# Performance work log

Measured on AMD Instinct MI355X. Metric: run time of the kernel, lower is better.

Reference implementation:

```python
import jax, jax.numpy as jnp
import numpy as np
import math

B, CIN, COUT, K, G, SD, H = 8, 512, 512, 3, 16, 512, 32
EPS = 1e-8


def _blur_kernel():
    k = jnp.array([1., 3., 3., 1.], dtype=jnp.float32)
    k = k[None, :] * k[:, None]
    k = k / k.sum()
    return k * 4.0  # upsample_factor ** 2


def setup_inputs() -> dict:
    key = jax.random.key(0)
    ks = jax.random.split(key, 10)
    return {
        "x": jax.random.normal(ks[0], (B, CIN, H, H), jnp.float32),
        "co": jax.random.uniform(ks[1], (1, CIN, CIN), jnp.float32),
        "style": jax.random.normal(ks[2], (B, 2 * SD), jnp.float32),
        "noise": jax.random.normal(ks[3], (B, 1, 2 * H, 2 * H), jnp.float32),
        "W": jax.random.normal(ks[4], (1, COUT, CIN, K, K), jnp.float32),
        "mb_w": jax.random.normal(ks[5], (G, SD), jnp.float32),
        "mb_b": jnp.ones((G,), jnp.float32),
        "mod_w": jax.random.normal(ks[6], (CIN, SD), jnp.float32),
        "mod_b": jnp.ones((CIN,), jnp.float32),
        "cluster": jax.random.normal(ks[7], (G, CIN), jnp.float32),
        "gate": -jnp.ones((1,), jnp.float32),
        "tmpr": -2.0 * jnp.ones((1,), jnp.float32),
        "noise_weight": jnp.zeros((1,), jnp.float32),
        "flr_bias": jnp.zeros((COUT,), jnp.float32),
    }


def _l2norm(x, axis):
    n = jnp.linalg.norm(x, axis=axis, keepdims=True)
    return x / jnp.maximum(n, 1e-12)


def reference(x, co, style, noise, W, mb_w, mb_b, mod_w, mod_b,
              cluster, gate, tmpr, noise_weight, flr_bias):
    scale = 1.0 / math.sqrt(CIN * K * K)   # GroupModulatedConv2d.scale
    lin_scale = 1.0 / math.sqrt(SD)        # EqualLinear scale (lr_mul=1)

    t = jax.nn.sigmoid(tmpr) * 5.0
    g = jax.nn.sigmoid(gate)
    S = jax.nn.sigmoid((co - g) * 50.0)                    # (1,Cin,Cin)
    cl = jax.nn.softmax(t * cluster, axis=0)               # (G,Cin)
    loss1 = jnp.sum((cl.T @ cl - jax.lax.stop_gradient(S)) ** 2)
    loss2 = jnp.sum((jnp.float32(CIN * CIN / G) - jnp.sum(S)) ** 2)
    grouped = jax.lax.stop_gradient(jnp.round(jax.nn.softmax(cl * 500.0, axis=0))) + 1e-6

    s1, s2 = style[:, :SD], style[:, SD:]
    style_base = (s1 @ (mb_w * lin_scale).T + mb_b)[:, :, None]   # (B,G,1)
    st = (s2 @ (mod_w * lin_scale).T + mod_b)[:, None, :]         # (B,1,Cin)
    tmp = _l2norm(grouped[None] * st, axis=2)                     # (B,G,Cin)
    st = jnp.sum(tmp * style_base, axis=1)                        # (B,Cin)

    w = scale * W * st[:, None, :, None, None]                    # (B,Cout,Cin,K,K)
    demod = jax.lax.rsqrt(jnp.sum(w * w, axis=(2, 3, 4)) + EPS)   # (B,Cout)
    w = w * demod[:, :, None, None, None]

    # conv_transpose2d(stride=2, pad=0, groups=B) == per-sample conv with
    # lhs_dilation=2, padding=K-1, spatially-flipped kernel.
    wf = w[:, :, :, ::-1, ::-1]

    def per_sample(xi, wi):  # xi (Cin,h,w), wi (Cout,Cin,K,K)
        return jax.lax.conv_general_dilated(
            xi[None], wi, window_strides=(1, 1),
            padding=((K - 1, K - 1), (K - 1, K - 1)), lhs_dilation=(2, 2),
            dimension_numbers=('NCHW', 'OIHW', 'NCHW'))[0]

    out = jax.vmap(per_sample)(x, wf)                             # (B,Cout,65,65)

    # Blur: upfirdn2d, pad=(1,1), depthwise 4x4 symmetric FIR kernel.
    bk = _blur_kernel()
    kdw = jnp.broadcast_to(bk[None, None], (COUT, 1, 4, 4))
    out = jax.lax.conv_general_dilated(
        out, kdw, (1, 1), ((1, 1), (1, 1)), feature_group_count=COUT,
        dimension_numbers=('NCHW', 'OIHW', 'NCHW'))                # (B,Cout,64,64)

    # Correlation of base weights (detached, fed to next layer as `co`).
    wflat = W.reshape(COUT, -1)
    wn = _l2norm(wflat, axis=1)
    co_out = jax.lax.stop_gradient((wn @ wn.T)[None])              # (1,Cout,Cout)

    # NoiseInjection + FusedLeakyReLU
    out = out + noise_weight * noise
    out = jax.nn.leaky_relu(out + flr_bias[None, :, None, None], 0.2) * math.sqrt(2.0)
    return out, co_out, loss1, loss2
```

## Files before the change

kernel.cpp:

```cpp
#include <hip/hip_runtime.h>
#include <hip/hip_bf16.h>

#define NB 8
#define LIN_SCALE 0.044194173824159216f
#define SCALE 0.014731391274719736f

typedef __attribute__((ext_vector_type(8))) short short8;
typedef __attribute__((ext_vector_type(4))) float floatx4;

static constexpr size_t O_XS   = 0;
static constexpr size_t O_OUT1 = 9469952;
static constexpr size_t O_WRT  = 44081152;
static constexpr size_t O_WB   = 48799744;
static constexpr size_t O_PG   = 53518336;
static constexpr size_t O_WSQ  = 61906944;
static constexpr size_t O_CL   = 62955520;
static constexpr size_t O_GR   = O_CL + 32768;
static constexpr size_t O_SB   = O_GR + 32768;
static constexpr size_t O_ST0  = O_SB + 1024;
static constexpr size_t O_STS  = O_ST0 + 16384;
static constexpr size_t O_ST2  = O_STS + 16384;
static constexpr size_t O_WNI  = O_ST2 + 16384;
static constexpr size_t O_DM   = O_WNI + 2048;
static constexpr size_t O_ACC  = O_DM + 16384;

static constexpr size_t OUT_CO = 16777216;
static constexpr size_t OUT_L  = 17039360;

__device__ const int c_ylim[4] = {33,33,32,32};
__device__ const int c_xlim[4] = {33,32,33,32};
__device__ const int c_ntap[4] = {4,2,2,1};
__device__ const int c_tap0[4] = {0,4,6,8};
__device__ const int c_nmb[4]  = {69,66,66,64};
__device__ const int c_cnt[4]  = {276,264,264,256};
__device__ const int c_dy[9] = {-1,-1,0,0, -1,0, 0,0, 0};
__device__ const int c_dx[9] = {-1,0,-1,0, 0,0, -1,0, 0};
__device__ const int c_ky[9] = {2,2,0,0, 2,0, 1,1, 1};
__device__ const int c_kx[9] = {2,0,2,0, 1,1, 2,0, 1};
__device__ const long c_poff[4] = {0, 4460544, 8785920, 13111296};

__device__ __forceinline__ float wave_red(float v) {
#pragma unroll
  for (int s = 32; s > 0; s >>= 1) v += __shfl_down(v, s);
  return v;
}

__device__ __forceinline__ void gl_lds16(const void* g, void* l) {
  __builtin_amdgcn_global_load_lds((const __attribute__((address_space(1))) void*)g,
                                   (__attribute__((address_space(3))) void*)l, 16, 0, 0);
}

__device__ __forceinline__ unsigned short bf16b(float f) {
  union { __hip_bfloat16 h; unsigned short u; } cv;
  cv.h = __float2bfloat16(f);
  return cv.u;
}

__device__ __forceinline__ float bfu(unsigned short u) {
  union { float f; unsigned u32; } c; c.u32 = ((unsigned)u) << 16; return c.f;
}

__device__ __forceinline__ int xcd_chunk(int lb, int cnt) {
  const int q = cnt >> 3, r = cnt & 7;
  const int c = lb & 7, i = lb >> 3;
  return (c < r) ? c*(q+1) + i : r*(q+1) + (c - r)*q + i;
}

__global__ __launch_bounds__(256) void k_big1(const float* __restrict__ W,
    float* __restrict__ wsq, float* __restrict__ wni,
    __hip_bfloat16* __restrict__ wrt, unsigned short* __restrict__ wb,
    const float* __restrict__ style, const float* __restrict__ mod_w,
    const float* __restrict__ mod_b, float* __restrict__ st0,
    const float* __restrict__ co, const float* __restrict__ gate,
    const float* __restrict__ cluster, const float* __restrict__ tmpr,
    const float* __restrict__ mb_w, const float* __restrict__ mb_b,
    float* __restrict__ gr, float* __restrict__ sb,
    float* __restrict__ pacc, __hip_bfloat16* __restrict__ xs) {
  __shared__ float sh[8192];
  __shared__ float extra[8];
  const int bid = blockIdx.x, tid = threadIdx.x;
  const int lane = tid & 63, wv = tid >> 6;
  if (bid < 512) {
    const int o = bid;
    for (int j = tid; j < 4608; j += 256) sh[j] = W[(size_t)o*4608 + j];
    __syncthreads();
    float tot = 0.f;
#pragma unroll
    for (int half = 0; half < 2; half++) {
      const int i = tid + half*256;
      float s = 0.f;
#pragma unroll
      for (int k = 0; k < 9; k++) { float w = sh[i*9 + k]; s = fmaf(w, w, s); }
      wsq[o*512 + i] = s; tot += s;
#pragma unroll
      for (int tp = 0; tp < 9; tp++)
        wrt[((size_t)tp*512 + o)*512 + i] = __float2bfloat16(sh[i*9 + c_ky[tp]*3 + c_kx[tp]]);
    }
    for (int j = tid; j < 4608; j += 256) wb[(size_t)o*4608 + j] = bf16b(sh[j]);
    tot = wave_red(tot);
    if (lane == 0) extra[wv] = tot;
    __syncthreads();
    if (tid == 0) wni[o] = 1.f / fmaxf(sqrtf(extra[0]+extra[1]+extra[2]+extra[3]), 1e-12f);
  } else if (bid < 576) {
    const int b = (bid - 512) >> 3, oc = (bid - 512) & 7;
    sh[tid] = style[b*1024 + 512 + tid];
    sh[tid + 256] = style[b*1024 + 768 + tid];
    __syncthreads();
#pragma unroll
    for (int rr = 0; rr < 16; rr++) {
      const int c = oc*64 + wv*16 + rr;
      const float* mw = mod_w + (size_t)c*512;
      float acc = 0.f;
#pragma unroll
      for (int it = 0; it < 8; it++) acc = fmaf(mw[lane + 64*it], sh[lane + 64*it], acc);
      acc = wave_red(acc);
      if (lane == 0) st0[b*512 + c] = acc*LIN_SCALE + mod_b[c];
    }
  } else if (bid < 1088) {
    const int i = bid - 576;
    const float tt = 5.f / (1.f + expf(-tmpr[0]));
    const float gg = 1.f / (1.f + expf(-gate[0]));
    for (int j = tid; j < 512; j += 256) {
      float v[16]; float m = -1e30f;
#pragma unroll
      for (int g = 0; g < 16; g++) { v[g] = tt * cluster[g*512 + j]; m = fmaxf(m, v[g]); }
      float s = 0.f;
#pragma unroll
      for (int g = 0; g < 16; g++) { v[g] = expf(v[g] - m); s += v[g]; }
      float inv = 1.f / s;
#pragma unroll
      for (int g = 0; g < 16; g++) sh[g*512 + j] = v[g] * inv;
    }
    __syncthreads();
    float cli[16];
#pragma unroll
    for (int k = 0; k < 16; k++) cli[k] = sh[k*512 + i];
    float p1 = 0.f, p2 = 0.f;
    for (int j = tid; j < 512; j += 256) {
      float d = 0.f;
#pragma unroll
      for (int k = 0; k < 16; k++) d = fmaf(cli[k], sh[k*512 + j], d);
      float S = 1.f / (1.f + expf(-50.f*(co[i*512 + j] - gg)));
      float e = d - S;
      p1 = fmaf(e, e, p1); p2 += S;
    }
    p1 = wave_red(p1); p2 = wave_red(p2);
    if (lane == 0) { extra[wv] = p1; extra[4 + wv] = p2; }
    __syncthreads();
    if (tid == 0)  pacc[i]       = extra[0]+extra[1]+extra[2]+extra[3];
    if (tid == 64) pacc[512 + i] = extra[4]+extra[5]+extra[6]+extra[7];
  } else if (bid == 1088) {
    const float tt = 5.f / (1.f + expf(-tmpr[0]));
#pragma unroll
    for (int h = 0; h < 2; h++) {
      const int c = tid + h*256;
      float v[16]; float m = -1e30f;
#pragma unroll
      for (int g = 0; g < 16; g++) { v[g] = tt * cluster[g*512 + c]; m = fmaxf(m, v[g]); }
      float s = 0.f;
#pragma unroll
      for (int g = 0; g < 16; g++) { v[g] = expf(v[g] - m); s += v[g]; }
      float inv = 1.f / s;
      float clv[16]; float m2 = -1e30f;
#pragma unroll
      for (int g = 0; g < 16; g++) { clv[g] = v[g]*inv; m2 = fmaxf(m2, 500.f*clv[g]); }
      float s2 = 0.f; float e2[16];
#pragma unroll
      for (int g = 0; g < 16; g++) { e2[g] = expf(500.f*clv[g] - m2); s2 += e2[g]; }
      float i2 = 1.f / s2;
#pragma unroll
      for (int g = 0; g < 16; g++) gr[g*512 + c] = rintf(e2[g]*i2) + 1e-6f;
    }
    for (int task = wv; task < 128; task += 4) {
      int b = task >> 4, g = task & 15;
      const float* s1 = style + b*1024;
      const float* mw = mb_w + g*512;
      float acc = 0.f;
#pragma unroll
      for (int it = 0; it < 8; it++) acc = fmaf(s1[lane + 64*it], mw[lane + 64*it], acc);
      acc = wave_red(acc);
      if (lane == 0) sb[b*16 + g] = acc*LIN_SCALE + mb_b[g];
    }
  } else {
    const int id0 = (bid - 1089)*256 + tid;
    const float4 z = make_float4(0.f, 0.f, 0.f, 0.f);
    float4* xq = (float4*)xs;
#pragma unroll
    for (int it = 0; it < 22; ++it) {
      const int id = id0 + it*3072;
      const int c = id & 63;
      const int pb = id >> 6;
      const int b = pb / 132;
      const int pix = pb - b*132;
      int y, xx;
      if (pix < 34)       { y = 0;        xx = pix; }
      else if (pix < 68)  { y = 33;       xx = pix - 34; }
      else if (pix < 100) { y = pix - 67; xx = 0; }
      else                { y = pix - 99; xx = 33; }
      xq[((size_t)(b*34 + y)*34 + xx)*64 + c] = z;
    }
  }
}

__global__ __launch_bounds__(256) void k_big2(const float* __restrict__ st0,
    const float* __restrict__ gr, const float* __restrict__ sb,
    const float* __restrict__ wsq, float* __restrict__ dm,
    const float* __restrict__ x, __hip_bfloat16* __restrict__ xs,
    const float* __restrict__ pacc, float* __restrict__ out_tail) {
  __shared__ float L[64*65];
  __shared__ float red[16][4];
  __shared__ float inv[16];
  __shared__ float sbb[16];
  const int tid = threadIdx.x;
  const int lane = tid & 63, wv = tid >> 6;

  if (blockIdx.x == 1088) {
    float a = pacc[tid] + pacc[tid + 256];
    float b2 = pacc[512 + tid] + pacc[768 + tid];
    a = wave_red(a); b2 = wave_red(b2);
    if (lane == 0) { red[0][wv] = a; red[1][wv] = b2; }
    __syncthreads();
    if (tid == 0) {
      float p1 = red[0][0]+red[0][1]+red[0][2]+red[0][3];
      float p2 = red[1][0]+red[1][1]+red[1][2]+red[1][3];
      out_tail[0] = p1;
      float d = 16384.f - p2;
      out_tail[1] = d*d;
    }
    return;
  }

  const int b = (blockIdx.x < 64) ? (blockIdx.x >> 3) : ((blockIdx.x - 64) >> 7);
  float s0 = st0[b*512 + tid], s1 = st0[b*512 + 256 + tid];
  float g0[16], g1[16];
#pragma unroll
  for (int g = 0; g < 16; g++) { g0[g] = gr[g*512 + tid]; g1[g] = gr[g*512 + 256 + tid]; }
#pragma unroll
  for (int g = 0; g < 16; g++) {
    float a = g0[g]*s0, c = g1[g]*s1;
    float p = wave_red(a*a + c*c);
    if (lane == 0) red[g][wv] = p;
  }
  if (tid < 16) sbb[tid] = sb[b*16 + tid];
  __syncthreads();
  if (tid < 16) {
    float ttn = red[tid][0] + red[tid][1] + red[tid][2] + red[tid][3];
    inv[tid] = 1.f / fmaxf(sqrtf(ttn), 1e-12f);
  }
  __syncthreads();
  float f0 = 0.f, f1 = 0.f;
#pragma unroll
  for (int g = 0; g < 16; g++) {
    float w = inv[g]*sbb[g];
    f0 = fmaf(g0[g], w, f0); f1 = fmaf(g1[g], w, f1);
  }
  const float sn0 = s0*f0, sn1 = s1*f1;

  if (blockIdx.x < 64) {
    const int oc = blockIdx.x & 7;
    L[tid] = sn0*sn0;
    L[tid + 256] = sn1*sn1;
    __syncthreads();
#pragma unroll
    for (int rr = 0; rr < 16; rr++) {
      const int o = oc*64 + wv*16 + rr;
      const float* wp = wsq + (size_t)o*512;
      float acc = 0.f;
#pragma unroll
      for (int it = 0; it < 8; it++) acc = fmaf(wp[lane + 64*it], L[lane + 64*it], acc);
      acc = wave_red(acc);
      if (lane == 0) dm[b*512 + o] = rsqrtf((1.0f/4608.0f)*acc + 1e-8f);
    }
    return;
  }

  L[tid] = sn0*SCALE;
  L[tid + 256] = sn1*SCALE;
  __syncthreads();
  const int id = blockIdx.x - 64;
  const int p0 = ((id >> 3) & 15) * 64;
  const int i0 = (id & 7) * 64;
  const int iw2 = (tid & 31) * 2, pw = tid >> 5;
  const float sv0 = L[i0 + iw2];
  const float sv1 = L[i0 + iw2 + 1];
  __syncthreads();
  const int cg = (tid & 15) * 4, ir = tid >> 4;
  const float* xp = x + ((size_t)b*512 + i0)*1024 + p0;
  float4 xv[4];
#pragma unroll
  for (int ii = 0; ii < 4; ii++) {
    const int i = ir + 16*ii;
    xv[ii] = *(const float4*)(xp + (size_t)i*1024 + cg);
  }
#pragma unroll
  for (int ii = 0; ii < 4; ii++) {
    const int i = ir + 16*ii;
    L[i*65 + cg + 0] = xv[ii].x;
    L[i*65 + cg + 1] = xv[ii].y;
    L[i*65 + cg + 2] = xv[ii].z;
    L[i*65 + cg + 3] = xv[ii].w;
  }
  __syncthreads();
#pragma unroll
  for (int pp = 0; pp < 8; pp++) {
    const int po = pw + 8*pp;
    const int pix = p0 + po;
    const int y = pix >> 5, xq = pix & 31;
    ushort2 w;
    w.x = bf16b(L[iw2*65 + po] * sv0);
    w.y = bf16b(L[(iw2+1)*65 + po] * sv1);
    *(ushort2*)((unsigned short*)xs + (((size_t)b*34 + (y+1))*34 + (xq+1))*512 + i0 + iw2) = w;
  }
}

__global__ __launch_bounds__(256, 3) void k_mfma(
    const __hip_bfloat16* __restrict__ xs, const __hip_bfloat16* __restrict__ wrt,
    __hip_bfloat16* __restrict__ out1, const __hip_bfloat16* __restrict__ wb,
    float* __restrict__ pgram) {
  __shared__ __hip_bfloat16 smem[24576];
  const int fid = blockIdx.x;
  const int tid = threadIdx.x;
  const int lane = tid & 63, wv = tid >> 6;
  const int wm = (wv >> 1) << 6, wn = (wv & 1) << 6;
  const int col16 = lane & 15, quad = lane >> 4;
  const int colp = col16 ^ ((col16 >> 2) & 1);
  const int soff = (quad ^ (col16 & 3)) << 3;

  int aoff[4], boff[4];
#pragma unroll
  for (int t = 0; t < 4; t++) {
    aoff[t] = (wm + t*16 + colp)*32 + soff;
    boff[t] = 4096 + (wn + t*16 + colp)*32 + soff;
  }
  floatx4 acc[4][4];
#pragma unroll
  for (int i = 0; i < 4; i++)
#pragma unroll
    for (int j = 0; j < 4; j++) acc[i][j] = (floatx4){0.f, 0.f, 0.f, 0.f};

  if (fid >= 276 && fid < 404) {
    const int g = xcd_chunk(fid - 276, 128);
    const int m0 = (g & 3) * 128, n0 = ((g >> 2) & 3) * 128;
    const long kz = (long)(g >> 4) * 576;
    long abase[2], bbase[2]; int ldso[2];
#pragma unroll
    for (int r = 0; r < 2; r++) {
      const int idx = r*256 + tid;
      const int rowp = idx >> 2;
      const int row = rowp ^ ((rowp >> 2) & 1);
      const int kc = (((idx & 3) ^ (row & 3)) << 3);
      abase[r] = (long)(m0 + row)*4608 + kz + kc;
      bbase[r] = (long)(n0 + row)*4608 + kz + kc;
      ldso[r] = idx << 3;
    }
#define STAGE_GRAM(s_, lo_) do { \
      const int kk_ = (s_) << 5; \
      gl_lds16(wb + (abase[0] + kk_), smem + (lo_) + ldso[0]); \
      gl_lds16(wb + (abase[1] + kk_), smem + (lo_) + ldso[1]); \
      gl_lds16(wb + (bbase[0] + kk_), smem + (lo_) + 4096 + ldso[0]); \
      gl_lds16(wb + (bbase[1] + kk_), smem + (lo_) + 4096 + ldso[1]); \
    } while (0)
    STAGE_GRAM(0, 0);
    STAGE_GRAM(1, 8192);
    int loC = 0, loS = 16384;
    for (int s = 0; s < 18; ++s) {
      if (s + 1 < 18) asm volatile("s_waitcnt vmcnt(4)\n\ts_barrier" ::: "memory");
      else            asm volatile("s_waitcnt vmcnt(0)\n\ts_barrier" ::: "memory");
      if (s + 2 < 18) STAGE_GRAM(s + 2, loS);
      short8 af[4], bfr[4];
#pragma unroll
      for (int t = 0; t < 4; t++) {
        af[t]  = *(const short8*)(smem + loC + aoff[t]);
        bfr[t] = *(const short8*)(smem + loC + boff[t]);
      }
      __builtin_amdgcn_s_setprio(1);
#pragma unroll
      for (int i = 0; i < 4; i++)
#pragma unroll
        for (int j = 0; j < 4; j++)
          acc[i][j] = __builtin_amdgcn_mfma_f32_16x16x32_bf16(af[i], bfr[j], acc[i][j], 0, 0, 0);
      __builtin_amdgcn_s_setprio(0);
      loC = (loC == 16384) ? 0 : loC + 8192;
      loS = (loS == 16384) ? 0 : loS + 8192;
    }
    float* pg = pgram + (size_t)(g >> 4) * 262144;
#pragma unroll
    for (int i = 0; i < 4; i++)
#pragma unroll
      for (int j = 0; j < 4; j++) {
        const int m = m0 + wm + i*16 + (quad << 2);
        const int n = n0 + wn + j*16 + col16;
#pragma unroll
        for (int r = 0; r < 4; r++) pg[(size_t)(m + r)*512 + n] = acc[i][j][r];
      }
    return;
  }

  int cls, lb;
  if (fid < 276)      { cls = 0; lb = fid; }
  else if (fid < 668) { cls = 1; lb = fid - 404; }
  else if (fid < 932) { cls = 2; lb = fid - 668; }
  else                { cls = 3; lb = fid - 932; }
  const int lg = xcd_chunk(lb, c_cnt[cls]);
  const int mb = lg >> 2, nb = lg & 3;
  const int xlim = c_xlim[cls];
  const int npix = c_ylim[cls] * xlim;
  const int M = NB * npix;
  const int m0 = mb * 128, n0 = nb * 128;
  const int t0 = c_tap0[cls];
  const int ntap = c_ntap[cls];

  long abase[2], bbase[2]; int ldso[2];
#pragma unroll
  for (int r = 0; r < 2; r++) {
    const int idx = r*256 + tid;
    const int rowp = idx >> 2;
    const int row = rowp ^ ((rowp >> 2) & 1);
    const int kc = (((idx & 3) ^ (row & 3)) << 3);
    int rm = m0 + row; if (rm >= M) rm = 0;
    const int b = rm / npix; const int rem = rm - b*npix;
    const int yy = rem / xlim; const int xx = rem - yy*xlim;
    abase[r] = ((long)(b*34 + yy + 1)*34 + (xx + 1))*512 + kc;
    bbase[r] = ((long)(t0*512 + n0 + row))*512 + kc;
    ldso[r] = idx << 3;
  }

  const int nst = ntap << 4;
#define STAGE_CONV(s_, lo_) do { \
    const int tap_ = t0 + ((s_) >> 4); \
    const long adel_ = (long)((c_dy[tap_]*34 + c_dx[tap_])*512); \
    const long bdel_ = (long)((s_) >> 4) << 18; \
    const int kk_ = ((s_) & 15) << 5; \
    gl_lds16(xs + (abase[0] + adel_ + kk_), smem + (lo_) + ldso[0]); \
    gl_lds16(xs + (abase[1] + adel_ + kk_), smem + (lo_) + ldso[1]); \
    gl_lds16(wrt + (bbase[0] + bdel_ + kk_), smem + (lo_) + 4096 + ldso[0]); \
    gl_lds16(wrt + (bbase[1] + bdel_ + kk_), smem + (lo_) + 4096 + ldso[1]); \
  } while (0)
  STAGE_CONV(0, 0);
  STAGE_CONV(1, 8192);
  int loC = 0, loS = 16384;
  for (int s = 0; s < nst; ++s) {
    if (s + 1 < nst) asm volatile("s_waitcnt vmcnt(4)\n\ts_barrier" ::: "memory");
    else             asm volatile("s_waitcnt vmcnt(0)\n\ts_barrier" ::: "memory");
    if (s + 2 < nst) STAGE_CONV(s + 2, loS);
    short8 af[4], bfr[4];
#pragma unroll
    for (int t = 0; t < 4; t++) {
      af[t]  = *(const short8*)(smem + loC + aoff[t]);
      bfr[t] = *(const short8*)(smem + loC + boff[t]);
    }
    __builtin_amdgcn_s_setprio(1);
#pragma unroll
    for (int i = 0; i < 4; i++)
#pragma unroll
      for (int j = 0; j < 4; j++)
        acc[i][j] = __builtin_amdgcn_mfma_f32_16x16x32_bf16(af[i], bfr[j], acc[i][j], 0, 0, 0);
    __builtin_amdgcn_s_setprio(0);
    loC = (loC == 16384) ? 0 : loC + 8192;
    loS = (loS == 16384) ? 0 : loS + 8192;
  }

  __syncthreads();
  __hip_bfloat16* plane = out1 + c_poff[cls];
#pragma unroll
  for (int h = 0; h < 2; h++) {
    if ((wv & 1) == h) {
#pragma unroll
      for (int i = 0; i < 4; i++) {
        const int mrow = wm + i*16 + (quad << 2);
#pragma unroll
        for (int j = 0; j < 4; j++) {
          const int ncl = j*16 + col16;
          ushort4 v;
          v.x = bf16b(acc[i][j][0]); v.y = bf16b(acc[i][j][1]);
          v.z = bf16b(acc[i][j][2]); v.w = bf16b(acc[i][j][3]);
          *(ushort4*)(smem + ncl*138 + mrow) = v;
        }
      }
    }
    __syncthreads();
#pragma unroll
    for (int it = 0; it < 4; it++) {
      const int c = it*256 + tid;
      const int ol = c >> 4, ml = (c & 15) << 3;
      const int mg = m0 + ml;
      if (mg < M) {
        const ushort4 v = *(const ushort4*)(smem + ol*138 + ml);
        *(ushort4*)(plane + (long)(n0 + h*64 + ol)*M + mg) = v;
      }
    }
    __syncthreads();
  }
}

__global__ __launch_bounds__(256) void k_blur(const __hip_bfloat16* __restrict__ out1,
    const float* __restrict__ dm, const float* __restrict__ noise,
    const float* __restrict__ nw, const float* __restrict__ fb, float* __restrict__ out,
    const float* __restrict__ pgram, const float* __restrict__ wni,
    float* __restrict__ co_out) {
  if (blockIdx.x < 256) {
    const int i4 = blockIdx.x*256 + threadIdx.x;
    float4 s = make_float4(0.f, 0.f, 0.f, 0.f);
#pragma unroll
    for (int z = 0; z < 8; z++) {
      const float4 v = ((const float4*)(pgram + (size_t)z*262144))[i4];
      s.x += v.x; s.y += v.y; s.z += v.z; s.w += v.w;
    }
    const float wm = wni[i4 >> 7];
    const float4 wn4 = ((const float4*)wni)[i4 & 127];
    float4 o;
    o.x = s.x*wm*wn4.x; o.y = s.y*wm*wn4.y; o.z = s.z*wm*wn4.z; o.w = s.w*wm*wn4.w;
    ((float4*)co_out)[i4] = o;
    return;
  }
  const int bo = blockIdx.x - 256;
  const int b = bo >> 9, o = bo & 511;
  __shared__ unsigned short L[65 * 68];
  __shared__ float Hs[67 * 64];
  const int tid = threadIdx.x;
  const unsigned short* p0 = (const unsigned short*)out1 + 0        + (long)o * 8712 + b * 1089;
  const unsigned short* p1 = (const unsigned short*)out1 + 4460544  + (long)o * 8448 + b * 1056;
  const unsigned short* p2 = (const unsigned short*)out1 + 8785920  + (long)o * 8448 + b * 1056;
  const unsigned short* p3 = (const unsigned short*)out1 + 13111296 + (long)o * 8192 + b * 1024;
  for (int m = tid; m < 65; m += 256) { L[m*68 + 0] = 0; L[m*68 + 66] = 0; }
  if (tid < 64) { Hs[tid] = 0.f; Hs[66*64 + tid] = 0.f; }
  for (int e = tid; e < 1089; e += 256) { int y = e / 33, x = e - 33*y; L[(2*y)*68 + 2*x + 1] = p0[e]; }
  for (int e2 = tid; e2 < 528; e2 += 256) {
    const int e = e2*2; const int y = e >> 5, x = e & 31;
    const ushort2 u = *(const ushort2*)(p1 + e);
    L[(2*y)*68 + 2*x + 2] = u.x; L[(2*y)*68 + 2*x + 4] = u.y;
  }
  for (int e = tid; e < 1056; e += 256) { int y = e / 33, x = e - 33*y; L[(2*y+1)*68 + 2*x + 1] = p2[e]; }
  for (int e2 = tid; e2 < 512; e2 += 256) {
    const int e = e2*2; const int y = e >> 5, x = e & 31;
    const ushort2 u = *(const ushort2*)(p3 + e);
    L[(2*y+1)*68 + 2*x + 2] = u.x; L[(2*y+1)*68 + 2*x + 4] = u.y;
  }
  __syncthreads();
  for (int e = tid; e < 4160; e += 256) {
    const int m = e >> 6, q = e & 63;
    const unsigned short* row = L + m*68 + q;
    Hs[(m+1)*64 + q] = 0.25f * (bfu(row[0]) + bfu(row[3])) + 0.75f * (bfu(row[1]) + bfu(row[2]));
  }
  __syncthreads();
  const float dmv = dm[bo];
  const float nwv = nw[0];
  const float bv = fb[o];
  const int qx = (tid & 15) << 2;
  const int py = tid >> 4;
  float* op = out + ((size_t)bo << 12);
  const float* npl = noise + ((size_t)b << 12);
#pragma unroll
  for (int pp = 0; pp < 4; pp++) {
    const int P = py + (pp << 4);
    const float4 h0 = *(const float4*)(Hs + (P    )*64 + qx);
    const float4 h1 = *(const float4*)(Hs + (P + 1)*64 + qx);
    const float4 h2 = *(const float4*)(Hs + (P + 2)*64 + qx);
    const float4 h3 = *(const float4*)(Hs + (P + 3)*64 + qx);
    const float4 n4 = *(const float4*)(npl + P*64 + qx);
    float4 ov;
    float s;
    s = 0.25f*(h0.x + h3.x) + 0.75f*(h1.x + h2.x);
    ov.x = fmaf(dmv, s, fmaf(nwv, n4.x, bv)); ov.x = (ov.x >= 0.f ? ov.x : 0.2f*ov.x) * 1.4142135623730951f;
    s = 0.25f*(h0.y + h3.y) + 0.75f*(h1.y + h2.y);
    ov.y = fmaf(dmv, s, fmaf(nwv, n4.y, bv)); ov.y = (ov.y >= 0.f ? ov.y : 0.2f*ov.y) * 1.4142135623730951f;
    s = 0.25f*(h0.z + h3.z) + 0.75f*(h1.z + h2.z);
    ov.z = fmaf(dmv, s, fmaf(nwv, n4.z, bv)); ov.z = (ov.z >= 0.f ? ov.z : 0.2f*ov.z) * 1.4142135623730951f;
    s = 0.25f*(h0.w + h3.w) + 0.75f*(h1.w + h2.w);
    ov.w = fmaf(dmv, s, fmaf(nwv, n4.w, bv)); ov.w = (ov.w >= 0.f ? ov.w : 0.2f*ov.w) * 1.4142135623730951f;
    *(float4*)(op + P*64 + qx) = ov;
  }
}

extern "C" void kernel_launch(void* const* d_in, const int* in_sizes, int n_in,
                              void* d_out, int out_size, void* d_ws, size_t ws_size,
                              hipStream_t stream) {
  const float* x       = (const float*)d_in[0];
  const float* co      = (const float*)d_in[1];
  const float* style   = (const float*)d_in[2];
  const float* noise   = (const float*)d_in[3];
  const float* W       = (const float*)d_in[4];
  const float* mb_w    = (const float*)d_in[5];
  const float* mb_b    = (const float*)d_in[6];
  const float* mod_w   = (const float*)d_in[7];
  const float* mod_b   = (const float*)d_in[8];
  const float* cluster = (const float*)d_in[9];
  const float* gate    = (const float*)d_in[10];
  const float* tmpr    = (const float*)d_in[11];
  const float* nw      = (const float*)d_in[12];
  const float* fb      = (const float*)d_in[13];
  float* out = (float*)d_out;
  char* ws = (char*)d_ws;

  __hip_bfloat16* xs   = (__hip_bfloat16*)(ws + O_XS);
  __hip_bfloat16* out1 = (__hip_bfloat16*)(ws + O_OUT1);
  __hip_bfloat16* wrt  = (__hip_bfloat16*)(ws + O_WRT);
  __hip_bfloat16* wb   = (__hip_bfloat16*)(ws + O_WB);
  float* pgram = (float*)(ws + O_PG);
  float* wsq = (float*)(ws + O_WSQ);
  float* gr  = (float*)(ws + O_GR);
  float* sb  = (float*)(ws + O_SB);
  float* st0 = (float*)(ws + O_ST0);
  float* wni = (float*)(ws + O_WNI);
  float* dm  = (float*)(ws + O_DM);
  float* pacc = (float*)(ws + O_STS);

  k_big1<<<1101, 256, 0, stream>>>(W, wsq, wni, wrt, (unsigned short*)wb,
                                   style, mod_w, mod_b, st0, co, gate,
                                   cluster, tmpr, mb_w, mb_b, gr, sb, pacc, xs);
  k_big2<<<1089, 256, 0, stream>>>(st0, gr, sb, wsq, dm, x, xs, pacc, out + OUT_L);
  k_mfma<<<1188, 256, 0, stream>>>(xs, wrt, out1, wb, pgram);
  k_blur<<<4352, 256, 0, stream>>>(out1, dm, noise, nw, fb, out, pgram, wni, out + OUT_CO);
}
```

Measured before the change: 239.5 us.

## Compute weight Gram from transposed wrt buffer, drop separate wb copy

```diff
diff --git a/kernel.cpp b/kernel.cpp
--- a/kernel.cpp
+++ b/kernel.cpp
@@ -68,7 +68,7 @@
 
 __global__ __launch_bounds__(256) void k_big1(const float* __restrict__ W,
     float* __restrict__ wsq, float* __restrict__ wni,
-    __hip_bfloat16* __restrict__ wrt, unsigned short* __restrict__ wb,
+    __hip_bfloat16* __restrict__ wrt,
     const float* __restrict__ style, const float* __restrict__ mod_w,
     const float* __restrict__ mod_b, float* __restrict__ st0,
     const float* __restrict__ co, const float* __restrict__ gate,
@@ -96,7 +96,6 @@
       for (int tp = 0; tp < 9; tp++)
         wrt[((size_t)tp*512 + o)*512 + i] = __float2bfloat16(sh[i*9 + c_ky[tp]*3 + c_kx[tp]]);
     }
-    for (int j = tid; j < 4608; j += 256) wb[(size_t)o*4608 + j] = bf16b(sh[j]);
     tot = wave_red(tot);
     if (lane == 0) extra[wv] = tot;
     __syncthreads();
@@ -315,8 +314,7 @@
 
 __global__ __launch_bounds__(256, 3) void k_mfma(
     const __hip_bfloat16* __restrict__ xs, const __hip_bfloat16* __restrict__ wrt,
-    __hip_bfloat16* __restrict__ out1, const __hip_bfloat16* __restrict__ wb,
-    float* __restrict__ pgram) {
+    __hip_bfloat16* __restrict__ out1, float* __restrict__ pgram) {
   __shared__ __hip_bfloat16 smem[24576];
   const int fid = blockIdx.x;
   const int tid = threadIdx.x;
@@ -338,10 +336,11 @@
 #pragma unroll
     for (int j = 0; j < 4; j++) acc[i][j] = (floatx4){0.f, 0.f, 0.f, 0.f};
 
-  if (fid >= 276 && fid < 404) {
-    const int g = xcd_chunk(fid - 276, 128);
-    const int m0 = (g & 3) * 128, n0 = ((g >> 2) & 3) * 128;
-    const long kz = (long)(g >> 4) * 576;
+  if (fid >= 276 && fid < 324) {
+    const int g = xcd_chunk(fid - 276, 48);
+    const int ts = g >> 4;
+    const int mn = g & 15;
+    const int m0 = (mn & 3) * 128, n0 = (mn >> 2) * 128;
     long abase[2], bbase[2]; int ldso[2];
 #pragma unroll
     for (int r = 0; r < 2; r++) {
@@ -349,41 +348,39 @@
       const int rowp = idx >> 2;
       const int row = rowp ^ ((rowp >> 2) & 1);
       const int kc = (((idx & 3) ^ (row & 3)) << 3);
-      abase[r] = (long)(m0 + row)*4608 + kz + kc;
-      bbase[r] = (long)(n0 + row)*4608 + kz + kc;
+      abase[r] = ((long)(ts*1536 + m0 + row))*512 + kc;
+      bbase[r] = ((long)(ts*1536 + n0 + row))*512 + kc;
       ldso[r] = idx << 3;
     }
 #define STAGE_GRAM(s_, lo_) do { \
-      const int kk_ = (s_) << 5; \
-      gl_lds16(wb + (abase[0] + kk_), smem + (lo_) + ldso[0]); \
-      gl_lds16(wb + (abase[1] + kk_), smem + (lo_) + ldso[1]); \
-      gl_lds16(wb + (bbase[0] + kk_), smem + (lo_) + 4096 + ldso[0]); \
-      gl_lds16(wb + (bbase[1] + kk_), smem + (lo_) + 4096 + ldso[1]); \
+      const long del_ = ((long)((s_) >> 4) << 18) + (((s_) & 15) << 5); \
+      gl_lds16(wrt + (abase[0] + del_), smem + (lo_) + ldso[0]); \
+      gl_lds16(wrt + (abase[1] + del_), smem + (lo_) + ldso[1]); \
+      gl_lds16(wrt + (bbase[0] + del_), smem + (lo_) + 4096 + ldso[0]); \
+      gl_lds16(wrt + (bbase[1] + del_), smem + (lo_) + 4096 + ldso[1]); \
     } while (0)
     STAGE_GRAM(0, 0);
     STAGE_GRAM(1, 8192);
     int loC = 0, loS = 16384;
-    for (int s = 0; s < 18; ++s) {
-      if (s + 1 < 18) asm volatile("s_waitcnt vmcnt(4)\n\ts_barrier" ::: "memory");
+    for (int s = 0; s < 48; ++s) {
+      if (s + 1 < 48) asm volatile("s_waitcnt vmcnt(4)\n\ts_barrier" ::: "memory");
       else            asm volatile("s_waitcnt vmcnt(0)\n\ts_barrier" ::: "memory");
-      if (s + 2 < 18) STAGE_GRAM(s + 2, loS);
+      if (s + 2 < 48) STAGE_GRAM(s + 2, loS);
       short8 af[4], bfr[4];
 #pragma unroll
       for (int t = 0; t < 4; t++) {
         af[t]  = *(const short8*)(smem + loC + aoff[t]);
         bfr[t] = *(const short8*)(smem + loC + boff[t]);
       }
-      __builtin_amdgcn_s_setprio(1);
 #pragma unroll
       for (int i = 0; i < 4; i++)
 #pragma unroll
         for (int j = 0; j < 4; j++)
           acc[i][j] = __builtin_amdgcn_mfma_f32_16x16x32_bf16(af[i], bfr[j], acc[i][j], 0, 0, 0);
-      __builtin_amdgcn_s_setprio(0);
       loC = (loC == 16384) ? 0 : loC + 8192;
       loS = (loS == 16384) ? 0 : loS + 8192;
     }
-    float* pg = pgram + (size_t)(g >> 4) * 262144;
+    float* pg = pgram + (size_t)ts * 262144;
 #pragma unroll
     for (int i = 0; i < 4; i++)
 #pragma unroll
@@ -398,9 +395,9 @@
 
   int cls, lb;
   if (fid < 276)      { cls = 0; lb = fid; }
-  else if (fid < 668) { cls = 1; lb = fid - 404; }
-  else if (fid < 932) { cls = 2; lb = fid - 668; }
-  else                { cls = 3; lb = fid - 932; }
+  else if (fid < 588) { cls = 1; lb = fid - 324; }
+  else if (fid < 852) { cls = 2; lb = fid - 588; }
+  else                { cls = 3; lb = fid - 852; }
   const int lg = xcd_chunk(lb, c_cnt[cls]);
   const int mb = lg >> 2, nb = lg & 3;
   const int xlim = c_xlim[cls];
@@ -449,13 +446,11 @@
       af[t]  = *(const short8*)(smem + loC + aoff[t]);
       bfr[t] = *(const short8*)(smem + loC + boff[t]);
     }
-    __builtin_amdgcn_s_setprio(1);
 #pragma unroll
     for (int i = 0; i < 4; i++)
 #pragma unroll
       for (int j = 0; j < 4; j++)
         acc[i][j] = __builtin_amdgcn_mfma_f32_16x16x32_bf16(af[i], bfr[j], acc[i][j], 0, 0, 0);
-    __builtin_amdgcn_s_setprio(0);
     loC = (loC == 16384) ? 0 : loC + 8192;
     loS = (loS == 16384) ? 0 : loS + 8192;
   }
@@ -502,7 +497,7 @@
     const int i4 = blockIdx.x*256 + threadIdx.x;
     float4 s = make_float4(0.f, 0.f, 0.f, 0.f);
 #pragma unroll
-    for (int z = 0; z < 8; z++) {
+    for (int z = 0; z < 3; z++) {
       const float4 v = ((const float4*)(pgram + (size_t)z*262144))[i4];
       s.x += v.x; s.y += v.y; s.z += v.z; s.w += v.w;
     }
@@ -595,7 +590,6 @@
   __hip_bfloat16* xs   = (__hip_bfloat16*)(ws + O_XS);
   __hip_bfloat16* out1 = (__hip_bfloat16*)(ws + O_OUT1);
   __hip_bfloat16* wrt  = (__hip_bfloat16*)(ws + O_WRT);
-  __hip_bfloat16* wb   = (__hip_bfloat16*)(ws + O_WB);
   float* pgram = (float*)(ws + O_PG);
   float* wsq = (float*)(ws + O_WSQ);
   float* gr  = (float*)(ws + O_GR);
@@ -605,10 +599,10 @@
   float* dm  = (float*)(ws + O_DM);
   float* pacc = (float*)(ws + O_STS);
 
-  k_big1<<<1101, 256, 0, stream>>>(W, wsq, wni, wrt, (unsigned short*)wb,
+  k_big1<<<1101, 256, 0, stream>>>(W, wsq, wni, wrt,
                                    style, mod_w, mod_b, st0, co, gate,
                                    cluster, tmpr, mb_w, mb_b, gr, sb, pacc, xs);
   k_big2<<<1089, 256, 0, stream>>>(st0, gr, sb, wsq, dm, x, xs, pacc, out + OUT_L);
-  k_mfma<<<1188, 256, 0, stream>>>(xs, wrt, out1, wb, pgram);
+  k_mfma<<<1108, 256, 0, stream>>>(xs, wrt, out1, pgram);
   k_blur<<<4352, 256, 0, stream>>>(out1, dm, noise, nw, fb, out, pgram, wni, out + OUT_CO);
 }
```

After: 237.5 us. Within noise of the previous version (-0.8%).
